# Performance work log

Hardware: AMD Instinct MI355X
Metric: run time of the kernel (lower is better)

Reference implementation:

```python
import jax, jax.numpy as jnp
import numpy as np

N_STEP = 3
N_INP = 256


def setup_inputs() -> dict:
    key = jax.random.key(0)
    ks = jax.random.split(key, 8)
    bs, L, n = 16, 128, N_INP
    s = 1.0 / np.sqrt(n)
    s2 = 1.0 / np.sqrt(2 * n)
    feat = jax.random.normal(ks[0], (bs, L, n), dtype=jnp.float32)
    mask = jnp.ones((bs, L), dtype=jnp.float32)
    # stacked per-step Linear params (torch Linear: y = x @ W.T + b)
    aggW = jax.random.uniform(ks[1], (N_STEP, n, n), minval=-s, maxval=s, dtype=jnp.float32)
    aggB = jax.random.uniform(ks[2], (N_STEP, n), minval=-s, maxval=s, dtype=jnp.float32)
    attnW = jax.random.uniform(ks[3], (N_STEP, n, 2 * n), minval=-s2, maxval=s2, dtype=jnp.float32)
    attnB = jax.random.uniform(ks[4], (N_STEP, n), minval=-s2, maxval=s2, dtype=jnp.float32)
    updW = jax.random.uniform(ks[5], (N_STEP, n, 2 * n), minval=-s2, maxval=s2, dtype=jnp.float32)
    updB = jax.random.uniform(ks[6], (N_STEP, n), minval=-s2, maxval=s2, dtype=jnp.float32)
    return {"feat": feat, "mask": mask, "aggW": aggW, "aggB": aggB,
            "attnW": attnW, "attnB": attnB, "updW": updW, "updB": updB}


def reference(feat, mask, aggW, aggB, attnW, attnB, updW, updB):
    bs, L, n = feat.shape
    hid = feat
    for i in range(N_STEP):
        hid = hid * mask[:, :, None]
        x = hid @ aggW[i].T + aggB[i]  # [b, s, n]
        # attn Linear on concat(x_s, x_j) splits into two matmuls
        W1 = attnW[i][:, :n]   # acts on x_s (sequence position)
        W2 = attnW[i][:, n:]   # acts on x_j (query node)
        p = x @ W1.T           # [b, s, n]
        q = x @ W2.T           # [b, j, n]
        # logits[b, j, s, c] = p[b, s, c] + q[b, j, c] + bias[c]
        logits = p[:, None, :, :] + q[:, :, None, :] + attnB[i]
        w = jax.nn.softmax(logits, axis=2)  # softmax over sequence dim per channel
        agg = jax.nn.sigmoid(jnp.einsum('bjsn,bsn->bjn', w, x))
        cat = jnp.concatenate([x, agg], axis=-1)  # [b, s, 2n]; dropout is identity (eval)
        hid = cat @ updW[i].T + updB[i]
    return hid
```

## Files before the change

### kernel.cpp

```cpp
#include <hip/hip_runtime.h>
#include <hip/hip_fp16.h>

#define NBLK  128
#define NPACK 192
#define NT    512
#define FPAD  16

typedef _Float16 h2_t  __attribute__((ext_vector_type(2)));
typedef _Float16 half8 __attribute__((ext_vector_type(8)));
typedef float    f32x4 __attribute__((ext_vector_type(4)));

#define AG_LD(p)    __hip_atomic_load((p), __ATOMIC_RELAXED, __HIP_MEMORY_SCOPE_AGENT)
#define AG_ST(p, v) __hip_atomic_store((p), (v), __ATOMIC_RELAXED, __HIP_MEMORY_SCOPE_AGENT)

__device__ __forceinline__ unsigned pkh(float a, float b) {
    const __half2 h = __floats2half2_rn(a, b);
    return __builtin_bit_cast(unsigned, h);
}
__device__ __forceinline__ float fdot2(unsigned w, unsigned a, float c) {
#if __has_builtin(__builtin_amdgcn_fdot2)
    return __builtin_amdgcn_fdot2(__builtin_bit_cast(h2_t, w),
                                  __builtin_bit_cast(h2_t, a), c, false);
#else
    const float2 fw = __half22float2(__builtin_bit_cast(__half2, w));
    const float2 fa = __half22float2(__builtin_bit_cast(__half2, a));
    return c + fw.x * fa.x + fw.y * fa.y;
#endif
}

__device__ __forceinline__ half8 ldw(const unsigned* p) {
    return __builtin_bit_cast(half8, *(const uint4*)p);
}
__device__ __forceinline__ f32x4 MF(half8 a, half8 b, f32x4 c) {
    return __builtin_amdgcn_mfma_f32_16x16x32_f16(a, b, c, 0, 0, 0);
}

__device__ __forceinline__ void bar_arrive(int n, unsigned* flags, int lid) {
    __syncthreads();
    if (threadIdx.x == 0)
        __hip_atomic_store(&flags[lid * FPAD], (unsigned)n, __ATOMIC_RELEASE,
                           __HIP_MEMORY_SCOPE_AGENT);
}
__device__ __forceinline__ void bar_wait_batch(int n, unsigned* flags, int b) {
    if (threadIdx.x < 8) {
        while ((int)__hip_atomic_load(&flags[(b * 8 + threadIdx.x) * FPAD],
                                      __ATOMIC_RELAXED,
                                      __HIP_MEMORY_SCOPE_AGENT) < n)
            __builtin_amdgcn_s_sleep(1);
    }
    __syncthreads();
}


__global__ __launch_bounds__(NT, 2) void pack_k(
    const float* __restrict__ aggW, const float* __restrict__ attnW,
    const float* __restrict__ updW, unsigned* __restrict__ WtH,
    unsigned* __restrict__ flags)
{
    __shared__ float Tl[64][65];
    const int bb = blockIdx.x, tid = threadIdx.x;
    const int m = bb >> 4, t = bb & 15, tr = t >> 2, tc = t & 3;
    const float* src; int stride, off;
    if (m < 3)      { src = aggW  + (size_t)m * 65536;        stride = 256; off = 0;   }
    else if (m < 6) { src = attnW + (size_t)(m - 3) * 131072; stride = 512; off = 0;   }
    else if (m < 9) { src = updW  + (size_t)(m - 6) * 131072; stride = 512; off = 0;   }
    else            { src = updW  + (size_t)(m - 9) * 131072; stride = 512; off = 256; }
    unsigned* dstu = WtH + (size_t)m * 32768;
    #pragma unroll
    for (int it = 0; it < 2; ++it) {
        const int j = it * 512 + tid, row = j >> 4, q = (j & 15) * 4;
        const float4 v = *(const float4*)(src + (size_t)(tr * 64 + row) * stride + off + tc * 64 + q);
        Tl[row][q + 0] = v.x; Tl[row][q + 1] = v.y;
        Tl[row][q + 2] = v.z; Tl[row][q + 3] = v.w;
    }
    if (bb == 0)
        for (int z = tid; z < 256 * FPAD; z += NT) flags[z] = 0u;
    __syncthreads();
    #pragma unroll
    for (int it = 0; it < 4; ++it) {
        const int j = it * 512 + tid, cl = j >> 5, pr = j & 31;
        const unsigned val = pkh(Tl[cl][pr * 2], Tl[cl][pr * 2 + 1]);
        const int C = tr * 64 + cl, P = tc * 32 + pr;
        size_t idx;
        if (m < 9) {
            const int ttn = C >> 4, lc = C & 15;
            const int kc = P >> 4, g = (P >> 2) & 3, sl = P & 3;
            idx = (size_t)((ttn * 8 + kc) * 256 + (g * 16 + lc) * 4 + sl);
        } else {
            idx = (size_t)(P >> 2) * 1024 + (size_t)C * 4 + (P & 3);
        }
        dstu[idx] = val;
    }
}

__device__ __forceinline__ float phaseB(int i, int b, int c, int rq, int tid,
                                        const float* __restrict__ part,
                                        const unsigned* __restrict__ WtH,
                                        const float* __restrict__ updB,
                                        float* S, unsigned* aggh, uint4* buf) {
    const float* pbase = part + (size_t)((i & 1) * 128 + b * 8 + rq * 4) * 768;
    float d[4], nn[4];
    #pragma unroll
    for (int j = 0; j < 4; ++j) {
        const float* pp = pbase + (size_t)j * 768;
        d[j]  = AG_LD(pp + c);
        nn[j] = AG_LD(pp + 256 + c);
    }
    S[rq * 256 + c] = (d[0] + d[1]) + (d[2] + d[3]);
    S[512 + rq * 256 + c] = (nn[0] + nn[1]) + (nn[2] + nn[3]);
    __syncthreads();
    if (tid < 128) {
        float sg[2];
        #pragma unroll
        for (int u = 0; u < 2; ++u) {
            const int cc = 2 * tid + u;
            const float dd = S[cc] + S[256 + cc];
            const float nv = S[512 + cc] + S[768 + cc];
            sg[u] = 1.f / (1.f + __expf(-(nv / dd)));
        }
        aggh[tid] = pkh(sg[0], sg[1]);
    }
    __syncthreads();
    const unsigned* Uq = WtH + (size_t)(9 + i) * 32768;
    const int g0 = rq * 16;
    float a0 = 0.f, a1 = 0.f, a2 = 0.f, a3 = 0.f;
    #pragma unroll
    for (int ph = 0; ph < 2; ++ph) {
        #pragma unroll
        for (int j = 0; j < 8; ++j) {
            const uint4 w = buf[j];
            if (ph < 1)
                buf[j] = *(const uint4*)(Uq + (size_t)(g0 + 8 + j) * 1024 + c * 4);
            const uint4 a = *(const uint4*)&aggh[(g0 + ph * 8 + j) * 4];
            a0 = fdot2(w.x, a.x, a0);
            a1 = fdot2(w.y, a.y, a1);
            a2 = fdot2(w.z, a.z, a2);
            a3 = fdot2(w.w, a.w, a3);
        }
    }
    const float au = (a0 + a1) + (a2 + a3);
    S[rq * 256 + c] = au;
    __syncthreads();
    return S[c] + S[256 + c] + updB[i * 256 + c];
}

__global__ __launch_bounds__(NT, 2) void main_k(
    const float* __restrict__ feat,
    const float* __restrict__ mask,
    const float* __restrict__ aggB,
    const float* __restrict__ updB,
    const unsigned* __restrict__ WtH,
    float* __restrict__ part,
    unsigned* flags,
    float* __restrict__ out)
{
    __shared__ __align__(16) float ldsf[6160];
    unsigned* hid_uu = (unsigned*)ldsf;
    unsigned* x_uu   = (unsigned*)ldsf + 2112;
    float*    accl   = ldsf + 4224;
    float*    S      = ldsf + 4480;
    unsigned* aggh   = (unsigned*)ldsf + 6016;
    float*    msk    = ldsf + 6144;

    const int bid = blockIdx.x;
    const int tid = threadIdx.x;
    const int c   = tid & 255;
    const int rq  = tid >> 8;
    const int wid = tid >> 6, lane = tid & 63;
    const int lr  = lane & 15, lg = lane >> 4;
    const int b   = 2 * (bid & 7) + ((bid >> 3) & 1);
    const int jj  = bid >> 4;
    const int lid = b * 8 + jj;
    const int row0 = b * 128 + jj * 16;

    #pragma unroll
    for (int it = 0; it < 4; ++it) {
        const int j = it * 512 + tid, r = j >> 7, pr = j & 127;
        const float2 f = *(const float2*)(feat + (size_t)(row0 + r) * 256 + pr * 2);
        const float mv = mask[row0 + r];
        hid_uu[r * 132 + pr] = pkh(f.x * mv, f.y * mv);
    }
    if (tid < 16) msk[tid] = mask[row0 + tid];
    __syncthreads();

    f32x4 xu0 = {}, xu1 = {};
    uint4 u2buf[8];

    for (int i = 0; i < 3; ++i) {
        if (i > 0) {
            const float accU = phaseB(i - 1, b, c, rq, tid, part, WtH, updB,
                                      S, aggh, u2buf);
            if (rq == 0) accl[c] = accU;
            __syncthreads();
            #pragma unroll
            for (int tt = 0; tt < 2; ++tt) {
                const int t = wid * 2 + tt;
                const f32x4 xa = tt ? xu1 : xu0;
                const float av = accl[t * 16 + lr];
                float hv[4], pv[4];
                #pragma unroll
                for (int q = 0; q < 4; ++q)
                    hv[q] = (xa[q] + av) * msk[lg * 4 + q];
                #pragma unroll
                for (int q = 0; q < 4; ++q) pv[q] = __shfl_xor(hv[q], 1);
                if (!(lr & 1)) {
                    const int p2 = t * 8 + (lr >> 1);
                    #pragma unroll
                    for (int q = 0; q < 4; ++q)
                        hid_uu[(lg * 4 + q) * 132 + p2] = pkh(hv[q], pv[q]);
                }
            }
            __syncthreads();
        }

        f32x4 xr0, xr1;

        {
            const unsigned* W0 = WtH + (size_t)i * 32768;
            half8 a[8];
            #pragma unroll
            for (int kc = 0; kc < 8; ++kc)
                a[kc] = ldw(hid_uu + lr * 132 + kc * 16 + lg * 4);
            #pragma unroll
            for (int tt = 0; tt < 2; ++tt) {
                const int t = wid * 2 + tt;
                f32x4 acc = {};
                #pragma unroll
                for (int kc = 0; kc < 8; ++kc)
                    acc = MF(a[kc], ldw(W0 + (size_t)(t * 8 + kc) * 256 + lane * 4), acc);
                const float bb = aggB[i * 256 + t * 16 + lr];
                #pragma unroll
                for (int q = 0; q < 4; ++q) acc[q] += bb;
                if (tt) xr1 = acc; else xr0 = acc;
                float pv[4];
                #pragma unroll
                for (int q = 0; q < 4; ++q) pv[q] = __shfl_xor(acc[q], 1);
                if (!(lr & 1)) {
                    const int p2 = t * 8 + (lr >> 1);
                    #pragma unroll
                    for (int q = 0; q < 4; ++q)
                        x_uu[(lg * 4 + q) * 132 + p2] = pkh(acc[q], pv[q]);
                }
            }
            __syncthreads();
        }

        {
            const unsigned* W1 = WtH + (size_t)(3 + i) * 32768;
            const unsigned* U1 = WtH + (size_t)(6 + i) * 32768;
            half8 a2[8];
            #pragma unroll
            for (int kc = 0; kc < 8; ++kc)
                a2[kc] = ldw(x_uu + lr * 132 + kc * 16 + lg * 4);
            float* pb = part + (size_t)((i & 1) * 128 + lid) * 768;
            #pragma unroll
            for (int tt = 0; tt < 2; ++tt) {
                const int t = wid * 2 + tt;
                f32x4 acc = {};
                #pragma unroll
                for (int kc = 0; kc < 8; ++kc)
                    acc = MF(a2[kc], ldw(W1 + (size_t)(t * 8 + kc) * 256 + lane * 4), acc);
                const f32x4 xa = tt ? xr1 : xr0;
                float d4 = 0.f, n4 = 0.f;
                #pragma unroll
                for (int q = 0; q < 4; ++q) {
                    const float e = __expf(acc[q]);
                    d4 += e;
                    n4 += e * xa[q];
                }
                d4 += __shfl_xor(d4, 16); d4 += __shfl_xor(d4, 32);
                n4 += __shfl_xor(n4, 16); n4 += __shfl_xor(n4, 32);
                if (lg == 0) {
                    const int cc = t * 16 + lr;
                    AG_ST(pb + cc, d4);
                    AG_ST(pb + 256 + cc, n4);
                }
            }
            bar_arrive(i + 1, flags, lid);
            #pragma unroll
            for (int tt = 0; tt < 2; ++tt) {
                const int t = wid * 2 + tt;
                f32x4 acc = {};
                #pragma unroll
                for (int kc = 0; kc < 8; ++kc)
                    acc = MF(a2[kc], ldw(U1 + (size_t)(t * 8 + kc) * 256 + lane * 4), acc);
                if (tt) xu1 = acc; else xu0 = acc;
            }
            {
                const unsigned* Uq = WtH + (size_t)(9 + i) * 32768;
                #pragma unroll
                for (int j = 0; j < 8; ++j)
                    u2buf[j] = *(const uint4*)(Uq + (size_t)(rq * 16 + j) * 1024 + c * 4);
            }
            bar_wait_batch(i + 1, flags, b);
        }
    }

    {
        const float accU = phaseB(2, b, c, rq, tid, part, WtH, updB, S, aggh, u2buf);
        if (rq == 0) accl[c] = accU;
        __syncthreads();
        #pragma unroll
        for (int tt = 0; tt < 2; ++tt) {
            const int t = wid * 2 + tt;
            const f32x4 xa = tt ? xu1 : xu0;
            const float av = accl[t * 16 + lr];
            #pragma unroll
            for (int q = 0; q < 4; ++q)
                out[(size_t)(row0 + lg * 4 + q) * 256 + t * 16 + lr] = xa[q] + av;
        }
    }
}

extern "C" void kernel_launch(void* const* d_in, const int* in_sizes, int n_in,
                              void* d_out, int out_size, void* d_ws, size_t ws_size,
                              hipStream_t stream) {
    const float* feat  = (const float*)d_in[0];
    const float* mask  = (const float*)d_in[1];
    const float* aggW  = (const float*)d_in[2];
    const float* aggB  = (const float*)d_in[3];
    const float* attnW = (const float*)d_in[4];
    const float* updW  = (const float*)d_in[6];
    const float* updB  = (const float*)d_in[7];

    unsigned* WtH = (unsigned*)d_ws;
    float* part = (float*)(WtH + 12 * 32768);
    unsigned* flags = (unsigned*)(part + 2 * 256 * 768);

    pack_k<<<NPACK, NT, 0, stream>>>(aggW, attnW, updW, WtH, flags);
    main_k<<<NBLK, NT, 0, stream>>>(feat, mask, aggB, updB, WtH, part, flags,
                                    (float*)d_out);
}
```

Measured before the change: 101.9 us.

## Split next-step aggregation matmul by linearity to overlap it with the grid barrier

The next step's aggW matmul is now split using linearity: W·(mask·(xu+av)) = mask·(W·xu + W·av). The large W·xu MFMA part runs before waiting on the cross-block batch barrier, hiding barrier latency behind useful work. The barrier-dependent part shrinks to a small fp16 dot-product matvec on the per-row aggregate vector, using extra packed aggW copies. The pack kernel gains more blocks and the workspace grows, and adding the two terms separately slightly changes rounding.

```diff
diff --git a/kernel.cpp b/kernel.cpp
--- a/kernel.cpp
+++ b/kernel.cpp
@@ -2,7 +2,7 @@
 #include <hip/hip_fp16.h>
 
 #define NBLK  128
-#define NPACK 192
+#define NPACK 224
 #define NT    512
 #define FPAD  16
 
@@ -61,10 +61,11 @@
     const int bb = blockIdx.x, tid = threadIdx.x;
     const int m = bb >> 4, t = bb & 15, tr = t >> 2, tc = t & 3;
     const float* src; int stride, off;
-    if (m < 3)      { src = aggW  + (size_t)m * 65536;        stride = 256; off = 0;   }
-    else if (m < 6) { src = attnW + (size_t)(m - 3) * 131072; stride = 512; off = 0;   }
-    else if (m < 9) { src = updW  + (size_t)(m - 6) * 131072; stride = 512; off = 0;   }
-    else            { src = updW  + (size_t)(m - 9) * 131072; stride = 512; off = 256; }
+    if (m < 3)       { src = aggW  + (size_t)m * 65536;         stride = 256; off = 0;   }
+    else if (m < 6)  { src = attnW + (size_t)(m - 3) * 131072;  stride = 512; off = 0;   }
+    else if (m < 9)  { src = updW  + (size_t)(m - 6) * 131072;  stride = 512; off = 0;   }
+    else if (m < 12) { src = updW  + (size_t)(m - 9) * 131072;  stride = 512; off = 256; }
+    else             { src = aggW  + (size_t)(m - 11) * 65536;  stride = 256; off = 0;   }
     unsigned* dstu = WtH + (size_t)m * 32768;
     #pragma unroll
     for (int it = 0; it < 2; ++it) {
@@ -183,75 +184,48 @@
     if (tid < 16) msk[tid] = mask[row0 + tid];
     __syncthreads();
 
+    f32x4 xr0, xr1;
     f32x4 xu0 = {}, xu1 = {};
+    f32x4 y0 = {}, y1 = {};
     uint4 u2buf[8];
 
+    {
+        const unsigned* W0 = WtH;
+        half8 a[8];
+        #pragma unroll
+        for (int kc = 0; kc < 8; ++kc)
+            a[kc] = ldw(hid_uu + lr * 132 + kc * 16 + lg * 4);
+        #pragma unroll
+        for (int tt = 0; tt < 2; ++tt) {
+            const int t = wid * 2 + tt;
+            f32x4 acc = {};
+            #pragma unroll
+            for (int kc = 0; kc < 8; ++kc)
+                acc = MF(a[kc], ldw(W0 + (size_t)(t * 8 + kc) * 256 + lane * 4), acc);
+            const float bb = aggB[t * 16 + lr];
+            #pragma unroll
+            for (int q = 0; q < 4; ++q) acc[q] += bb;
+            if (tt) xr1 = acc; else xr0 = acc;
+            float pv[4];
+            #pragma unroll
+            for (int q = 0; q < 4; ++q) pv[q] = __shfl_xor(acc[q], 1);
+            if (!(lr & 1)) {
+                const int p2 = t * 8 + (lr >> 1);
+                #pragma unroll
+                for (int q = 0; q < 4; ++q)
+                    x_uu[(lg * 4 + q) * 132 + p2] = pkh(acc[q], pv[q]);
+            }
+        }
+        __syncthreads();
+    }
+
     for (int i = 0; i < 3; ++i) {
-        if (i > 0) {
-            const float accU = phaseB(i - 1, b, c, rq, tid, part, WtH, updB,
-                                      S, aggh, u2buf);
-            if (rq == 0) accl[c] = accU;
-            __syncthreads();
-            #pragma unroll
-            for (int tt = 0; tt < 2; ++tt) {
-                const int t = wid * 2 + tt;
-                const f32x4 xa = tt ? xu1 : xu0;
-                const float av = accl[t * 16 + lr];
-                float hv[4], pv[4];
-                #pragma unroll
-                for (int q = 0; q < 4; ++q)
-                    hv[q] = (xa[q] + av) * msk[lg * 4 + q];
-                #pragma unroll
-                for (int q = 0; q < 4; ++q) pv[q] = __shfl_xor(hv[q], 1);
-                if (!(lr & 1)) {
-                    const int p2 = t * 8 + (lr >> 1);
-                    #pragma unroll
-                    for (int q = 0; q < 4; ++q)
-                        hid_uu[(lg * 4 + q) * 132 + p2] = pkh(hv[q], pv[q]);
-                }
-            }
-            __syncthreads();
-        }
-
-        f32x4 xr0, xr1;
-
-        {
-            const unsigned* W0 = WtH + (size_t)i * 32768;
-            half8 a[8];
-            #pragma unroll
-            for (int kc = 0; kc < 8; ++kc)
-                a[kc] = ldw(hid_uu + lr * 132 + kc * 16 + lg * 4);
-            #pragma unroll
-            for (int tt = 0; tt < 2; ++tt) {
-                const int t = wid * 2 + tt;
-                f32x4 acc = {};
-                #pragma unroll
-                for (int kc = 0; kc < 8; ++kc)
-                    acc = MF(a[kc], ldw(W0 + (size_t)(t * 8 + kc) * 256 + lane * 4), acc);
-                const float bb = aggB[i * 256 + t * 16 + lr];
-                #pragma unroll
-                for (int q = 0; q < 4; ++q) acc[q] += bb;
-                if (tt) xr1 = acc; else xr0 = acc;
-                float pv[4];
-                #pragma unroll
-                for (int q = 0; q < 4; ++q) pv[q] = __shfl_xor(acc[q], 1);
-                if (!(lr & 1)) {
-                    const int p2 = t * 8 + (lr >> 1);
-                    #pragma unroll
-                    for (int q = 0; q < 4; ++q)
-                        x_uu[(lg * 4 + q) * 132 + p2] = pkh(acc[q], pv[q]);
-                }
-            }
-            __syncthreads();
-        }
-
+        half8 a2[8];
+        #pragma unroll
+        for (int kc = 0; kc < 8; ++kc)
+            a2[kc] = ldw(x_uu + lr * 132 + kc * 16 + lg * 4);
         {
             const unsigned* W1 = WtH + (size_t)(3 + i) * 32768;
-            const unsigned* U1 = WtH + (size_t)(6 + i) * 32768;
-            half8 a2[8];
-            #pragma unroll
-            for (int kc = 0; kc < 8; ++kc)
-                a2[kc] = ldw(x_uu + lr * 132 + kc * 16 + lg * 4);
             float* pb = part + (size_t)((i & 1) * 128 + lid) * 768;
             #pragma unroll
             for (int tt = 0; tt < 2; ++tt) {
@@ -277,6 +251,9 @@
                 }
             }
             bar_arrive(i + 1, flags, lid);
+        }
+        {
+            const unsigned* U1 = WtH + (size_t)(6 + i) * 32768;
             #pragma unroll
             for (int tt = 0; tt < 2; ++tt) {
                 const int t = wid * 2 + tt;
@@ -286,28 +263,106 @@
                     acc = MF(a2[kc], ldw(U1 + (size_t)(t * 8 + kc) * 256 + lane * 4), acc);
                 if (tt) xu1 = acc; else xu0 = acc;
             }
+        }
+
+        if (i < 2) {
+            #pragma unroll
+            for (int tt = 0; tt < 2; ++tt) {
+                const int t = wid * 2 + tt;
+                const f32x4 xa = tt ? xu1 : xu0;
+                float pv[4];
+                #pragma unroll
+                for (int q = 0; q < 4; ++q) pv[q] = __shfl_xor(xa[q], 1);
+                if (!(lr & 1)) {
+                    const int p2 = t * 8 + (lr >> 1);
+                    #pragma unroll
+                    for (int q = 0; q < 4; ++q)
+                        hid_uu[(lg * 4 + q) * 132 + p2] = pkh(xa[q], pv[q]);
+                }
+            }
+            __syncthreads();
+            const unsigned* Wn = WtH + (size_t)(i + 1) * 32768;
+            half8 a3[8];
+            #pragma unroll
+            for (int kc = 0; kc < 8; ++kc)
+                a3[kc] = ldw(hid_uu + lr * 132 + kc * 16 + lg * 4);
+            #pragma unroll
+            for (int tt = 0; tt < 2; ++tt) {
+                const int t = wid * 2 + tt;
+                f32x4 acc = {};
+                #pragma unroll
+                for (int kc = 0; kc < 8; ++kc)
+                    acc = MF(a3[kc], ldw(Wn + (size_t)(t * 8 + kc) * 256 + lane * 4), acc);
+                if (tt) y1 = acc; else y0 = acc;
+            }
+        }
+
+        {
+            const unsigned* Uq = WtH + (size_t)(9 + i) * 32768;
+            #pragma unroll
+            for (int j = 0; j < 8; ++j)
+                u2buf[j] = *(const uint4*)(Uq + (size_t)(rq * 16 + j) * 1024 + c * 4);
+        }
+        bar_wait_batch(i + 1, flags, b);
+
+        const float accU = phaseB(i, b, c, rq, tid, part, WtH, updB,
+                                  S, aggh, u2buf);
+
+        if (i < 2) {
+            if (rq == 0) accl[c] = accU;
+            __syncthreads();
+            if (tid < 128) aggh[tid] = pkh(accl[2 * tid], accl[2 * tid + 1]);
+            __syncthreads();
             {
-                const unsigned* Uq = WtH + (size_t)(9 + i) * 32768;
-                #pragma unroll
-                for (int j = 0; j < 8; ++j)
-                    u2buf[j] = *(const uint4*)(Uq + (size_t)(rq * 16 + j) * 1024 + c * 4);
-            }
-            bar_wait_batch(i + 1, flags, b);
-        }
-    }
-
-    {
-        const float accU = phaseB(2, b, c, rq, tid, part, WtH, updB, S, aggh, u2buf);
-        if (rq == 0) accl[c] = accU;
-        __syncthreads();
-        #pragma unroll
-        for (int tt = 0; tt < 2; ++tt) {
-            const int t = wid * 2 + tt;
-            const f32x4 xa = tt ? xu1 : xu0;
-            const float av = accl[t * 16 + lr];
-            #pragma unroll
-            for (int q = 0; q < 4; ++q)
-                out[(size_t)(row0 + lg * 4 + q) * 256 + t * 16 + lr] = xa[q] + av;
+                const unsigned* Vq = WtH + (size_t)(12 + i) * 32768;
+                const int g0 = rq * 16;
+                float v0 = 0.f, v1 = 0.f, v2 = 0.f, v3 = 0.f;
+                #pragma unroll
+                for (int j = 0; j < 16; ++j) {
+                    const uint4 w = *(const uint4*)(Vq + (size_t)(g0 + j) * 1024 + c * 4);
+                    const uint4 a = *(const uint4*)&aggh[(g0 + j) * 4];
+                    v0 = fdot2(w.x, a.x, v0);
+                    v1 = fdot2(w.y, a.y, v1);
+                    v2 = fdot2(w.z, a.z, v2);
+                    v3 = fdot2(w.w, a.w, v3);
+                }
+                S[rq * 256 + c] = (v0 + v1) + (v2 + v3);
+            }
+            __syncthreads();
+            #pragma unroll
+            for (int tt = 0; tt < 2; ++tt) {
+                const int t = wid * 2 + tt;
+                const f32x4 ya = tt ? y1 : y0;
+                const float vv = S[t * 16 + lr] + S[256 + t * 16 + lr];
+                const float bb = aggB[(i + 1) * 256 + t * 16 + lr];
+                f32x4 xnew;
+                #pragma unroll
+                for (int q = 0; q < 4; ++q)
+                    xnew[q] = msk[lg * 4 + q] * (ya[q] + vv) + bb;
+                if (tt) xr1 = xnew; else xr0 = xnew;
+                float pv[4];
+                #pragma unroll
+                for (int q = 0; q < 4; ++q) pv[q] = __shfl_xor(xnew[q], 1);
+                if (!(lr & 1)) {
+                    const int p2 = t * 8 + (lr >> 1);
+                    #pragma unroll
+                    for (int q = 0; q < 4; ++q)
+                        x_uu[(lg * 4 + q) * 132 + p2] = pkh(xnew[q], pv[q]);
+                }
+            }
+            __syncthreads();
+        } else {
+            if (rq == 0) accl[c] = accU;
+            __syncthreads();
+            #pragma unroll
+            for (int tt = 0; tt < 2; ++tt) {
+                const int t = wid * 2 + tt;
+                const f32x4 xa = tt ? xu1 : xu0;
+                const float av = accl[t * 16 + lr];
+                #pragma unroll
+                for (int q = 0; q < 4; ++q)
+                    out[(size_t)(row0 + lg * 4 + q) * 256 + t * 16 + lr] = xa[q] + av;
+            }
         }
     }
 }
@@ -324,7 +379,7 @@
     const float* updB  = (const float*)d_in[7];
 
     unsigned* WtH = (unsigned*)d_ws;
-    float* part = (float*)(WtH + 12 * 32768);
+    float* part = (float*)(WtH + 14 * 32768);
     unsigned* flags = (unsigned*)(part + 2 * 256 * 768);
 
     pack_k<<<NPACK, NT, 0, stream>>>(aggW, attnW, updW, WtH, flags);
```

Result: slower. 119.1 us (+16.8%).
